# Kernel tuning notes

Measured on AMD Instinct MI355X. Metric: run time of the kernel, lower is better.

Reference implementation:

```python
import jax, jax.numpy as jnp
import numpy as np

NUM_ELMT = 64
INPUT_DIM = 16
BOUND = 50.0
MESH_RATIO = 1.2
N_POINTS = 1_048_576


def _build_mesh():
    m = NUM_ELMT
    one_step = BOUND * (MESH_RATIO - 1.0) / (MESH_RATIO ** (m / 2) - 1.0)
    idx = np.arange(-m / 2, m / 2 + 1)
    mesh = (MESH_RATIO ** np.abs(idx) - 1.0) / (MESH_RATIO - 1.0) * one_step * np.sign(idx)
    mesh_norm = (mesh + BOUND) / (2.0 * BOUND)
    mesh_norm = np.concatenate([[0.0], mesh_norm[1:-1], [1.0]]).astype(np.float32)
    elmt_size = (mesh_norm[1:] - mesh_norm[:-1]).astype(np.float32)
    return jnp.asarray(mesh_norm), jnp.asarray(elmt_size)


def setup_inputs() -> dict:
    key = jax.random.key(0)
    k1, k2 = jax.random.split(key)
    x = jax.random.uniform(k1, (N_POINTS, INPUT_DIM), jnp.float32, minval=-BOUND, maxval=BOUND)
    pdj = jnp.ones((N_POINTS, 1), jnp.float32)
    sldj = jnp.zeros((N_POINTS, 1), jnp.float32)
    log_p = 0.1 * jax.random.normal(k2, (NUM_ELMT - 1, INPUT_DIM), jnp.float32)
    mesh_norm, elmt_size = _build_mesh()
    return {"x": x, "pdj": pdj, "sldj": sldj, "log_p": log_p,
            "mesh_norm": mesh_norm, "elmt_size": elmt_size}


def _normalize_pdf(log_p, elmt_size):
    # elmt_size: (M,) -> (M,1) column, log_p: (M-1, D)
    es = elmt_size[:, None]
    ep = jnp.exp(log_p)
    px = ep * (es[:-1] + es[1:]) / 2.0
    px = ep * (1.0 - es[0]) / jnp.sum(px, axis=0, keepdims=True)
    p0 = jnp.ones((1, log_p.shape[1]), log_p.dtype)
    pdf_norm = jnp.concatenate([p0, px, p0], axis=0)            # (M+1, D)
    cell = (pdf_norm[:-1] + pdf_norm[1:]) / 2.0 * es            # (M, D)
    # F_ref[i] = sum(cell[:i]); single cumsum instead of the O(M^2) torch loop
    F_ref = jnp.concatenate([jnp.zeros_like(p0), jnp.cumsum(cell, axis=0)[:-1]], axis=0)  # (M, D)
    return pdf_norm, F_ref


def reference(x, pdj, sldj, log_p, mesh_norm, elmt_size):
    pdf_norm, F_ref = _normalize_pdf(log_p, elmt_size)
    xn = (x + BOUND) / (2.0 * BOUND)                            # (N, D) in [0,1]
    k = jnp.searchsorted(mesh_norm, xn, side='left')            # (N, D), torch right=False
    cover = (k != 0) & (k != NUM_ELMT + 1)
    k = jnp.clip(k, 1, NUM_ELMT)
    km1 = k - 1
    v1 = jnp.take_along_axis(pdf_norm, km1, axis=0)             # pdf at lower node
    v2 = jnp.take_along_axis(pdf_norm, k, axis=0)               # pdf at upper node
    xmodi = xn - mesh_norm[km1]                                 # offset inside element
    h = elmt_size[km1]                                          # element width
    F_pre = jnp.take_along_axis(F_ref, km1, axis=0)             # CDF at lower node
    y = jnp.where(cover, F_pre + xmodi * xmodi * 0.5 * (v2 - v1) / h + xmodi * v1, xn)
    abs_det = jnp.where(cover, xmodi * (v2 - v1) / h + v1, 1.0)
    pdj_out = pdj * jnp.prod(abs_det, axis=-1, keepdims=True)
    sldj_out = sldj + jnp.sum(jnp.log(abs_det), axis=-1, keepdims=True)
    x_out = y * 2.0 * BOUND - BOUND
    return (x_out, pdj_out, sldj_out)
```

## Files before the change

### kernel.cpp

```cpp
#include <hip/hip_runtime.h>
#include <math.h>


namespace {
constexpr int DIM = 16;
constexpr int ME  = 64;
constexpr float BOUNDF = 50.0f;
constexpr float K1      = 6.8164378f;
constexpr float INV_L2R = 3.8017840f;
constexpr int COEF_FLOATS = ME * 68;
constexpr int EP_BASE     = COEF_FLOATS - 63 * DIM;
}

__device__ __forceinline__ int imin(int a, int b) { return a < b ? a : b; }
__device__ __forceinline__ int imax(int a, int b) { return a > b ? a : b; }

__global__ __launch_bounds__(256) void nll_kernel(
    const float* __restrict__ x,
    const float* __restrict__ pdj,
    const float* __restrict__ sldj,
    const float* __restrict__ log_p,
    const float* __restrict__ mesh_norm,
    const float* __restrict__ elmt_size,
    float* __restrict__ out,
    int npts, int npairs)
{
  __shared__ __align__(16) float co[COEF_FLOATS];
  __shared__ float  s_mesh[ME + 1];
  __shared__ float2 s_pair[ME];
  __shared__ float  s_invh[ME];

  const int tid = threadIdx.x;

  if (tid <= ME) s_mesh[tid] = mesh_norm[tid];
  if (tid >= 128 && tid < 128 + ME) {
    const int j = tid - 128;
    s_invh[j] = 1.0f / (mesh_norm[j + 1] - mesh_norm[j]);
  }
  for (int i = tid; i < 63 * DIM; i += 256)
    co[EP_BASE + i] = __expf(log_p[i]);
  __syncthreads();

  if (tid < DIM) {
    const int d = tid;
    float ssum = 0.f;
    for (int j = 0; j < ME - 1; ++j)
      ssum += co[EP_BASE + j * DIM + d] * (s_mesh[j + 2] - s_mesh[j]);
    ssum *= 0.5f;
    const float scale = (1.0f - (s_mesh[1] - s_mesh[0])) / ssum;
    float F = 0.f, prev = 1.0f;
    for (int j = 0; j < ME; ++j) {
      const float cur = (j < ME - 1) ? co[EP_BASE + j * DIM + d] * scale : 1.0f;
      const float m = s_mesh[j];
      const float h = s_mesh[j + 1] - m;
      const float A = 0.5f * (cur - prev) * s_invh[j];
      const float B = fmaf(-2.0f * A, m, prev);
      const float D = fmaf(m, fmaf(m, A, -prev), F);
      *reinterpret_cast<float4*>(&co[j * 68 + 4 * d]) = make_float4(A, B, D, A + A);
      F = fmaf((prev + cur) * 0.5f, h, F);
      prev = cur;
    }
  } else if (tid >= 64 && tid < 64 + ME) {
    const int k = tid - 64;
    s_pair[k] = make_float2(s_mesh[k], s_mesh[k + 1]);
  }
  __syncthreads();

  const int tpg = gridDim.x * blockDim.x;
  const float4* __restrict__ x4 = reinterpret_cast<const float4*>(x);
  float4* __restrict__ out4 = reinterpret_cast<float4*>(out);
  const int np16 = npts * DIM;

  for (int t = blockIdx.x * blockDim.x + tid; t < npairs; t += tpg) {
    const int p = t >> 1;
    const int hh = t & 1;
    const float4 xa = x4[2 * t];
    const float4 xb = x4[2 * t + 1];
    const float vals[8] = {xa.x, xa.y, xa.z, xa.w, xb.x, xb.y, xb.z, xb.w};
    float yv[8];
    float prodq = 1.f;

#pragma unroll
    for (int j = 0; j < 8; ++j) {
      const int d = (hh << 3) + j;
      const float val = vals[j];
      const float xn = (val + BOUNDF) * 0.01f;
      const bool cover = (xn > 0.f) && (xn <= 1.f);

      const float tt = fabsf(val);
      const float u = fmaf(tt, K1, 1.0f);
      const float n = __log2f(u) * INV_L2R;
      int k = (val > 0.f) ? (32 + (int)ceilf(n)) : (32 - (int)floorf(n));
      k = imin(imax(k, 1), ME);

      const float2 pr = s_pair[k - 1];
      int km1 = (k - 1) + (xn > pr.y ? 1 : 0) - (xn <= pr.x ? 1 : 0);
      km1 = imin(imax(km1, 0), ME - 1);

      const float4 cf = *reinterpret_cast<const float4*>(&co[km1 * 68 + 4 * d]);
      float y  = fmaf(xn, fmaf(xn, cf.x, cf.y), cf.z);
      float dt = fmaf(xn, cf.w, cf.y);
      y  = cover ? y  : xn;
      dt = cover ? dt : 1.0f;
      yv[j] = fmaf(y, 2.0f * BOUNDF, -BOUNDF);
      prodq *= dt;
    }

    out4[2 * t]     = make_float4(yv[0], yv[1], yv[2], yv[3]);
    out4[2 * t + 1] = make_float4(yv[4], yv[5], yv[6], yv[7]);

    const float other = __shfl_xor(prodq, 1);
    const float full = prodq * other;
    if (hh == 0) out[np16 + p]        = pdj[p] * full;
    else         out[np16 + npts + p] = sldj[p] + __logf(full);
  }
}

extern "C" void kernel_launch(void* const* d_in, const int* in_sizes, int n_in,
                              void* d_out, int out_size, void* d_ws, size_t ws_size,
                              hipStream_t stream) {
  const float* x    = (const float*)d_in[0];
  const float* pdj  = (const float*)d_in[1];
  const float* sldj = (const float*)d_in[2];
  const float* lp   = (const float*)d_in[3];
  const float* mesh = (const float*)d_in[4];
  const float* es   = (const float*)d_in[5];
  float* out = (float*)d_out;

  const int npts   = in_sizes[0] / DIM;
  const int npairs = npts * 2;
  const int block  = 256;
  int grid = 2048;
  const int needed = (npairs + block - 1) / block;
  if (needed < grid) grid = needed;

  hipLaunchKernelGGL(nll_kernel, dim3(grid), dim3(block), 0, stream,
                     x, pdj, sldj, lp, mesh, es, out, npts, npairs);
}
```

Before: 36.07 us.

## Parallelize per-block coefficient setup with wave scans and process one point per thread

The per-block coefficient table setup moves from a serial 64-step loop in 16 threads to all 256 threads. Each wave handles 4 dimensions and uses shuffle reductions for the normalizer and shuffle prefix scans for the CDF. The main loop now gives one whole point (16 dims) to each thread instead of half a point, which removes the cross-lane shuffle for the product. The searchsorted correction step with neighbour mesh checks is dropped in favour of a single ceil(copysign) index formula. That shortens block prologue latency and per-element work, but it risks off-by-one bin errors near mesh nodes and gives each thread fewer loads in flight with more registers per thread.

```diff
diff --git a/kernel.cpp b/kernel.cpp
--- a/kernel.cpp
+++ b/kernel.cpp
@@ -12,107 +12,102 @@
 constexpr int EP_BASE     = COEF_FLOATS - 63 * DIM;
 }
 
-__device__ __forceinline__ int imin(int a, int b) { return a < b ? a : b; }
-__device__ __forceinline__ int imax(int a, int b) { return a > b ? a : b; }
-
 __global__ __launch_bounds__(256) void nll_kernel(
     const float* __restrict__ x,
     const float* __restrict__ pdj,
     const float* __restrict__ sldj,
     const float* __restrict__ log_p,
     const float* __restrict__ mesh_norm,
-    const float* __restrict__ elmt_size,
     float* __restrict__ out,
-    int npts, int npairs)
+    int npts)
 {
   __shared__ __align__(16) float co[COEF_FLOATS];
-  __shared__ float  s_mesh[ME + 1];
-  __shared__ float2 s_pair[ME];
-  __shared__ float  s_invh[ME];
+  __shared__ float s_mesh[ME + 1];
 
   const int tid = threadIdx.x;
 
   if (tid <= ME) s_mesh[tid] = mesh_norm[tid];
-  if (tid >= 128 && tid < 128 + ME) {
-    const int j = tid - 128;
-    s_invh[j] = 1.0f / (mesh_norm[j + 1] - mesh_norm[j]);
-  }
   for (int i = tid; i < 63 * DIM; i += 256)
     co[EP_BASE + i] = __expf(log_p[i]);
   __syncthreads();
 
-  if (tid < DIM) {
-    const int d = tid;
-    float ssum = 0.f;
-    for (int j = 0; j < ME - 1; ++j)
-      ssum += co[EP_BASE + j * DIM + d] * (s_mesh[j + 2] - s_mesh[j]);
-    ssum *= 0.5f;
-    const float scale = (1.0f - (s_mesh[1] - s_mesh[0])) / ssum;
-    float F = 0.f, prev = 1.0f;
-    for (int j = 0; j < ME; ++j) {
-      const float cur = (j < ME - 1) ? co[EP_BASE + j * DIM + d] * scale : 1.0f;
-      const float m = s_mesh[j];
-      const float h = s_mesh[j + 1] - m;
-      const float A = 0.5f * (cur - prev) * s_invh[j];
-      const float B = fmaf(-2.0f * A, m, prev);
-      const float D = fmaf(m, fmaf(m, A, -prev), F);
-      *reinterpret_cast<float4*>(&co[j * 68 + 4 * d]) = make_float4(A, B, D, A + A);
-      F = fmaf((prev + cur) * 0.5f, h, F);
-      prev = cur;
-    }
-  } else if (tid >= 64 && tid < 64 + ME) {
-    const int k = tid - 64;
-    s_pair[k] = make_float2(s_mesh[k], s_mesh[k + 1]);
+  const int wv = tid >> 6, lane = tid & 63;
+  float epv[4];
+#pragma unroll
+  for (int i = 0; i < 4; ++i)
+    epv[i] = (lane < 63) ? co[EP_BASE + lane * DIM + (4 * wv + i)] : 0.f;
+  const float mj  = s_mesh[lane];
+  const float mj1 = s_mesh[lane + 1];
+  const float mj2 = s_mesh[(lane + 2 > ME) ? ME : (lane + 2)];
+  const float es0 = s_mesh[1] - s_mesh[0];
+  __syncthreads();
+
+  const float h = mj1 - mj;
+#pragma unroll
+  for (int i = 0; i < 4; ++i) {
+    const int d = 4 * wv + i;
+    const float ep = epv[i];
+    float ss = (lane < 63) ? ep * (mj2 - mj) : 0.f;
+    ss += __shfl_xor(ss, 1);  ss += __shfl_xor(ss, 2);  ss += __shfl_xor(ss, 4);
+    ss += __shfl_xor(ss, 8);  ss += __shfl_xor(ss, 16); ss += __shfl_xor(ss, 32);
+    const float scale = (1.0f - es0) / (0.5f * ss);
+    const float cur = (lane < 63) ? ep * scale : 1.0f;
+    float prev = __shfl_up(cur, 1);
+    if (lane == 0) prev = 1.0f;
+    const float cell = (prev + cur) * 0.5f * h;
+    float v = cell, o;
+    o = __shfl_up(v, 1);  if (lane >= 1)  v += o;
+    o = __shfl_up(v, 2);  if (lane >= 2)  v += o;
+    o = __shfl_up(v, 4);  if (lane >= 4)  v += o;
+    o = __shfl_up(v, 8);  if (lane >= 8)  v += o;
+    o = __shfl_up(v, 16); if (lane >= 16) v += o;
+    o = __shfl_up(v, 32); if (lane >= 32) v += o;
+    const float F = v - cell;
+    const float A = 0.5f * (cur - prev) / h;
+    const float B = fmaf(-(A + A), mj, prev);
+    const float D = fmaf(mj, fmaf(mj, A, -prev), F);
+    *reinterpret_cast<float4*>(&co[lane * 68 + 4 * d]) = make_float4(A, B, D, A + A);
   }
   __syncthreads();
 
-  const int tpg = gridDim.x * blockDim.x;
+  const int stride = gridDim.x * blockDim.x;
   const float4* __restrict__ x4 = reinterpret_cast<const float4*>(x);
   float4* __restrict__ out4 = reinterpret_cast<float4*>(out);
   const int np16 = npts * DIM;
 
-  for (int t = blockIdx.x * blockDim.x + tid; t < npairs; t += tpg) {
-    const int p = t >> 1;
-    const int hh = t & 1;
-    const float4 xa = x4[2 * t];
-    const float4 xb = x4[2 * t + 1];
-    const float vals[8] = {xa.x, xa.y, xa.z, xa.w, xb.x, xb.y, xb.z, xb.w};
-    float yv[8];
-    float prodq = 1.f;
+  for (int p = blockIdx.x * blockDim.x + tid; p < npts; p += stride) {
+    float4 X[4];
+#pragma unroll
+    for (int q = 0; q < 4; ++q) X[q] = x4[4 * p + q];
+    const float* vals = reinterpret_cast<const float*>(X);
+    float yv[16];
+    float prod = 1.f;
 
 #pragma unroll
-    for (int j = 0; j < 8; ++j) {
-      const int d = (hh << 3) + j;
+    for (int j = 0; j < 16; ++j) {
       const float val = vals[j];
       const float xn = (val + BOUNDF) * 0.01f;
-      const bool cover = (xn > 0.f) && (xn <= 1.f);
-
-      const float tt = fabsf(val);
-      const float u = fmaf(tt, K1, 1.0f);
+      const float u = fmaf(fabsf(val), K1, 1.0f);
       const float n = __log2f(u) * INV_L2R;
-      int k = (val > 0.f) ? (32 + (int)ceilf(n)) : (32 - (int)floorf(n));
-      k = imin(imax(k, 1), ME);
-
-      const float2 pr = s_pair[k - 1];
-      int km1 = (k - 1) + (xn > pr.y ? 1 : 0) - (xn <= pr.x ? 1 : 0);
-      km1 = imin(imax(km1, 0), ME - 1);
-
-      const float4 cf = *reinterpret_cast<const float4*>(&co[km1 * 68 + 4 * d]);
+      const int k32 = (int)ceilf(copysignf(n, val));
+      int km1 = k32 + 31;
+      km1 = km1 < 0 ? 0 : (km1 > 63 ? 63 : km1);
+      const float4 cf = *reinterpret_cast<const float4*>(&co[km1 * 68 + 4 * j]);
       float y  = fmaf(xn, fmaf(xn, cf.x, cf.y), cf.z);
       float dt = fmaf(xn, cf.w, cf.y);
+      const bool cover = (xn > 0.f) && (xn <= 1.0f);
       y  = cover ? y  : xn;
       dt = cover ? dt : 1.0f;
       yv[j] = fmaf(y, 2.0f * BOUNDF, -BOUNDF);
-      prodq *= dt;
+      prod *= dt;
     }
 
-    out4[2 * t]     = make_float4(yv[0], yv[1], yv[2], yv[3]);
-    out4[2 * t + 1] = make_float4(yv[4], yv[5], yv[6], yv[7]);
-
-    const float other = __shfl_xor(prodq, 1);
-    const float full = prodq * other;
-    if (hh == 0) out[np16 + p]        = pdj[p] * full;
-    else         out[np16 + npts + p] = sldj[p] + __logf(full);
+    float4* o4 = &out4[4 * p];
+#pragma unroll
+    for (int q = 0; q < 4; ++q)
+      o4[q] = make_float4(yv[4 * q], yv[4 * q + 1], yv[4 * q + 2], yv[4 * q + 3]);
+    out[np16 + p]        = pdj[p] * prod;
+    out[np16 + npts + p] = sldj[p] + __logf(prod);
   }
 }
 
@@ -124,16 +119,14 @@
   const float* sldj = (const float*)d_in[2];
   const float* lp   = (const float*)d_in[3];
   const float* mesh = (const float*)d_in[4];
-  const float* es   = (const float*)d_in[5];
   float* out = (float*)d_out;
 
-  const int npts   = in_sizes[0] / DIM;
-  const int npairs = npts * 2;
-  const int block  = 256;
+  const int npts  = in_sizes[0] / DIM;
+  const int block = 256;
   int grid = 2048;
-  const int needed = (npairs + block - 1) / block;
+  const int needed = (npts + block - 1) / block;
   if (needed < grid) grid = needed;
 
   hipLaunchKernelGGL(nll_kernel, dim3(grid), dim3(block), 0, stream,
-                     x, pdj, sldj, lp, mesh, es, out, npts, npairs);
+                     x, pdj, sldj, lp, mesh, out, npts);
 }
```

Result: slower. 37.51 us (+4.0%).
